# Performance work log

Measured on AMD Instinct MI355X. Metric: run time of the kernel, lower is better.

The kernel has to match this reference:

```python
import jax, jax.numpy as jnp
import numpy as np

# model constants
D = 2048; D_INNER = 4096; H = 64; P = 64; N = 128; K = 4; CHUNK = 256
E = 8; TOPK = 2; I_EXP = 1024; I_SH = 4096
EPS = 1e-5; RES_MULT = 0.22
CONV_DIM = D_INNER + 2 * N  # n_groups=1


def rmsnorm(x, w, eps=EPS):
    var = jnp.mean(x * x, axis=-1, keepdims=True)
    return x * jax.lax.rsqrt(var + eps) * w


def segsum(x):
    # x: [..., L] -> [..., L, L] lower-triangular cumulative sums, -inf above diag
    L = x.shape[-1]
    cs = jnp.cumsum(x, axis=-1)
    d = cs[..., :, None] - cs[..., None, :]
    mask = jnp.tril(jnp.ones((L, L), dtype=bool))
    return jnp.where(mask, d, -jnp.inf)


def ssd(x, dt, A, Bm, Cm, chunk=CHUNK):
    # x:[b,s,h,p] dt:[b,s,h] A:[h] Bm/Cm:[b,s,n] (single group)
    b, S, h, p = x.shape
    n = Bm.shape[-1]
    nc = S // chunk
    xc = x.reshape(b, nc, chunk, h, p)
    dtc = dt.reshape(b, nc, chunk, h)
    Bc = Bm.reshape(b, nc, chunk, n)
    Cc = Cm.reshape(b, nc, chunk, n)
    dA = jnp.transpose(dtc * A, (0, 1, 3, 2))          # [b,c,h,l]
    dA_cum = jnp.cumsum(dA, axis=-1)                    # [b,c,h,l]
    xdt = xc * dtc[..., None]                           # [b,c,l,h,p]
    # intra-chunk (quadratic attention-like block)
    CB = jnp.einsum('bcln,bcsn->bcls', Cc, Bc)
    Lmat = jnp.exp(segsum(dA))                          # [b,c,h,l,s]
    Y = jnp.einsum('bcls,bchls,bcshp->bclhp', CB, Lmat, xdt)
    # per-chunk final states
    decay_states = jnp.exp(dA_cum[..., -1:] - dA_cum)   # [b,c,h,l]
    states = jnp.einsum('bcln,bchl,bclhp->bchpn', Bc, decay_states, xdt)
    # inter-chunk recurrence (small scan over nc chunks)
    chunk_decay = jnp.exp(dA_cum[..., -1])              # [b,c,h]
    dec_c = jnp.moveaxis(chunk_decay, 1, 0)             # [c,b,h]
    st_c = jnp.moveaxis(states, 1, 0)                   # [c,b,h,p,n]

    def step(carry, inp):
        dec, st = inp
        return carry * dec[..., None, None] + st, carry

    _, prev = jax.lax.scan(step, jnp.zeros_like(st_c[0]), (dec_c, st_c))
    prev = jnp.moveaxis(prev, 0, 1)                     # [b,c,h,p,n] state before each chunk
    out_decay = jnp.exp(jnp.transpose(dA_cum, (0, 1, 3, 2)))  # [b,c,l,h]
    Y = Y + jnp.einsum('bcln,bchpn->bclhp', Cc, prev) * out_decay[..., None]
    return Y.reshape(b, S, h, p)


def causal_conv_silu(u, w, bias):
    # u:[b,s,c], depthwise causal conv kernel w:[c,K]
    S = u.shape[1]
    up = jnp.pad(u, ((0, 0), (K - 1, 0), (0, 0)))
    y = sum(up[:, i:i + S, :] * w[:, i] for i in range(K)) + bias
    return jax.nn.silu(y)


def setup_inputs() -> dict:
    key = jax.random.key(0)
    ks = jax.random.split(key, 16)
    B, S = 1, 4096
    sc = 0.02
    return {
        'positions': jnp.arange(B * S, dtype=jnp.int32).reshape(B, S),
        'hidden_states': jax.random.normal(ks[0], (B, S, D), jnp.float32),
        'ln1_w': jnp.ones((D,), jnp.float32),
        'in_proj_w': jax.random.normal(ks[1], (D, 2 * D_INNER + 2 * N + H), jnp.float32) * sc,
        'conv_w': jax.random.normal(ks[2], (CONV_DIM, K), jnp.float32) * 0.2,
        'conv_b': jnp.zeros((CONV_DIM,), jnp.float32),
        'A_log': jnp.log(jax.random.uniform(ks[3], (H,), jnp.float32, 1.0, 16.0)),
        'dt_bias': jax.random.normal(ks[4], (H,), jnp.float32) * 0.5,
        'D_param': jnp.ones((H,), jnp.float32),
        'mamba_norm_w': jnp.ones((D_INNER,), jnp.float32),
        'out_proj_w': jax.random.normal(ks[5], (D_INNER, D), jnp.float32) * sc,
        'ln2_w': jnp.ones((D,), jnp.float32),
        'router_w': jax.random.normal(ks[6], (D, E), jnp.float32) * sc,
        'moe_w_gate_up': jax.random.normal(ks[7], (E, D, 2 * I_EXP), jnp.float32) * sc,
        'moe_w_down': jax.random.normal(ks[8], (E, I_EXP, D), jnp.float32) * sc,
        'shared_w_in': jax.random.normal(ks[9], (D, 2 * I_SH), jnp.float32) * sc,
        'shared_w_out': jax.random.normal(ks[10], (I_SH, D), jnp.float32) * sc,
    }


def reference(positions, hidden_states, ln1_w, in_proj_w, conv_w, conv_b, A_log,
              dt_bias, D_param, mamba_norm_w, out_proj_w, ln2_w, router_w,
              moe_w_gate_up, moe_w_down, shared_w_in, shared_w_out):
    B, S, _ = hidden_states.shape
    residual = hidden_states
    h = rmsnorm(hidden_states, ln1_w)
    # ---- Mamba2 mixer ----
    proj = h @ in_proj_w                                  # [B,S,2*Di+2N+H]
    z = proj[..., :D_INNER]
    xBC = proj[..., D_INNER:D_INNER + CONV_DIM]
    dt_raw = proj[..., D_INNER + CONV_DIM:]
    xBC = causal_conv_silu(xBC, conv_w, conv_b)
    x = xBC[..., :D_INNER].reshape(B, S, H, P)
    Bm = xBC[..., D_INNER:D_INNER + N]
    Cm = xBC[..., D_INNER + N:]
    dt = jax.nn.softplus(dt_raw + dt_bias)                # [B,S,H]
    A = -jnp.exp(A_log)                                   # [H]
    y = ssd(x, dt, A, Bm, Cm) + x * D_param[None, None, :, None]
    y = y.reshape(B, S, D_INNER)
    y = rmsnorm(y * jax.nn.silu(z), mamba_norm_w)         # gated RMSNorm
    mamba_out = y @ out_proj_w
    hidden = residual + mamba_out * RES_MULT
    residual = hidden
    # ---- MoE + shared MLP ----
    h2 = rmsnorm(hidden, ln2_w)
    ht = h2.reshape(-1, D)
    T = ht.shape[0]
    logits = ht @ router_w                                # [T,E]
    topv, topi = jax.lax.top_k(logits, TOPK)
    wts = jax.nn.softmax(topv, axis=-1)
    gates = jnp.zeros((T, E), ht.dtype).at[jnp.arange(T)[:, None], topi].set(wts)
    moe_out = jnp.zeros_like(ht)
    for e in range(E):
        gu = ht @ moe_w_gate_up[e]
        a = jax.nn.silu(gu[:, :I_EXP]) * gu[:, I_EXP:]
        moe_out = moe_out + gates[:, e:e + 1] * (a @ moe_w_down[e])
    gu = ht @ shared_w_in
    shared_out = (jax.nn.silu(gu[:, :I_SH]) * gu[:, I_SH:]) @ shared_w_out
    ff = (moe_out + shared_out).reshape(B, S, D)
    hidden = residual + ff * RES_MULT
    return (hidden, residual)
```

## Files before the change

### kernel.cpp

```cpp
#include <hip/hip_runtime.h>
#include <stdint.h>

typedef unsigned short u16;
typedef __attribute__((ext_vector_type(8))) __bf16 bf16x8;
typedef __attribute__((ext_vector_type(4))) float f32x4;

#define SEQ     4096
#define DMODEL  2048
#define DINNER  4096
#define NHEADS  64
#define HEADP   64
#define NSTATE  128
#define NCHUNK  16
#define CHUNKL  256
#define NPROJ   8512
#define NPROJP  8576
#define CONVDIM 4352
#define RESM    0.22f
#define MAXROWS 9216
#define MAXTILE 72

static __device__ __forceinline__ u16 f2bf(float f){
  union { float f; uint32_t u; } v; v.f = f;
  uint32_t r = v.u + 0x7fffu + ((v.u >> 16) & 1u);
  return (u16)(r >> 16);
}
static __device__ __forceinline__ float bf2f(u16 h){
  union { uint32_t u; float f; } v; v.u = ((uint32_t)h) << 16;
  return v.f;
}
static __device__ __forceinline__ float siluf(float x){ return x / (1.f + __expf(-x)); }

static __device__ __forceinline__ void gll16(const void* g, void* l) {
  __builtin_amdgcn_global_load_lds(
      (const __attribute__((address_space(1))) void*)g,
      (__attribute__((address_space(3))) void*)l, 16, 0, 0);
}

static __device__ __forceinline__ int swz_src_c8(int tid) {
  return ((((tid & 3) - ((tid >> 3) & 3) + 4) & 3) * 8);
}
static __device__ __forceinline__ int swz_rd_sl8(int fr, int g) {
  return (((g + ((fr >> 1) & 3)) & 3) * 8);
}

static __device__ __forceinline__ void decode_tile(
    int id, int NB, int MB, int G, int& bx, int& by)
{
  const int nwg = NB * MB;
  int sid = id;
  if (!(nwg & 7)) {
    const int cpx = nwg >> 3;
    sid = (id & 7) * cpx + (id >> 3);
  }
  const int gsz = MB * G;
  const int fullG = NB / G;
  const int fullCnt = fullG * gsz;
  if (sid < fullCnt) {
    const int grp = sid / gsz;
    const int r = sid - grp * gsz;
    const int q = r / G;
    by = q;
    bx = grp * G + (r - q * G);
  } else {
    const int rem = NB - fullG * G;
    const int r = sid - fullCnt;
    const int q = r / rem;
    by = q;
    bx = fullG * G + (r - q * rem);
  }
}

__global__ __launch_bounds__(256) void rmsnorm_split(
    const float* __restrict__ in, const float* __restrict__ w,
    u16* __restrict__ hi, u16* __restrict__ lo, int width)
{
  const int row = blockIdx.x;
  const float* x = in + (size_t)row * width;
  float ss = 0.f;
  for (int i = threadIdx.x * 4; i < width; i += 1024) {
    float4 v = *(const float4*)&x[i];
    ss += v.x*v.x + v.y*v.y + v.z*v.z + v.w*v.w;
  }
  #pragma unroll
  for (int off = 32; off > 0; off >>= 1) ss += __shfl_down(ss, off);
  __shared__ float red[4];
  if ((threadIdx.x & 63) == 0) red[threadIdx.x >> 6] = ss;
  __syncthreads();
  const float total = red[0] + red[1] + red[2] + red[3];
  const float scale = rsqrtf(total / (float)width + 1e-5f);
  u16* oh = hi + (size_t)row * width;
  u16* ol = lo + (size_t)row * width;
  for (int i = threadIdx.x * 4; i < width; i += 1024) {
    float4 v = *(const float4*)&x[i];
    float4 g = *(const float4*)&w[i];
    #pragma unroll
    for (int q = 0; q < 4; q++) {
      const float val = ((const float*)&v)[q] * scale * ((const float*)&g)[q];
      const u16 H = f2bf(val);
      oh[i+q] = H;
      ol[i+q] = f2bf(val - bf2f(H));
    }
  }
}

__global__ __launch_bounds__(256) void wconv_t(
    const float* __restrict__ W, u16* __restrict__ Bt, int K, int N)
{
  const size_t eo = (size_t)blockIdx.z * K * N;
  W += eo; Bt += eo;
  __shared__ float t[32][33];
  const int n0 = blockIdx.x * 32, k0 = blockIdx.y * 32;
  const int tx = threadIdx.x & 31, ty = threadIdx.x >> 5;
  #pragma unroll
  for (int r = 0; r < 32; r += 8)
    t[ty + r][tx] = W[(size_t)(k0 + ty + r) * N + n0 + tx];
  __syncthreads();
  #pragma unroll
  for (int r = 0; r < 32; r += 8)
    Bt[(size_t)(n0 + ty + r) * K + k0 + tx] = f2bf(t[tx][ty + r]);
}

__global__ __launch_bounds__(256) void wconv_t_glu(
    const float* __restrict__ W, u16* __restrict__ Bt, int K, int N, int H)
{
  const size_t eo = (size_t)blockIdx.z * K * N;
  W += eo; Bt += eo;
  __shared__ float t[32][33];
  const int n0 = blockIdx.x * 32, k0 = blockIdx.y * 32;
  const int tx = threadIdx.x & 31, ty = threadIdx.x >> 5;
  #pragma unroll
  for (int r = 0; r < 32; r += 8)
    t[ty + r][tx] = W[(size_t)(k0 + ty + r) * N + n0 + tx];
  __syncthreads();
  #pragma unroll
  for (int r = 0; r < 32; r += 8) {
    const int n = n0 + ty + r;
    const int orow = (n < H) ? (2 * n) : (2 * (n - H) + 1);
    Bt[(size_t)orow * K + k0 + tx] = f2bf(t[tx][ty + r]);
  }
}

__global__ __launch_bounds__(256) void wconv_t_split(
    const float* __restrict__ W, u16* __restrict__ Bth, u16* __restrict__ Btl, int K, int N)
{
  __shared__ float t[32][33];
  const int n0 = blockIdx.x * 32, k0 = blockIdx.y * 32;
  const int tx = threadIdx.x & 31, ty = threadIdx.x >> 5;
  #pragma unroll
  for (int r = 0; r < 32; r += 8)
    t[ty + r][tx] = W[(size_t)(k0 + ty + r) * N + n0 + tx];
  __syncthreads();
  #pragma unroll
  for (int r = 0; r < 32; r += 8) {
    const float val = t[tx][ty + r];
    const u16 H = f2bf(val);
    const size_t idx = (size_t)(n0 + ty + r) * K + k0 + tx;
    Bth[idx] = H;
    Btl[idx] = f2bf(val - bf2f(H));
  }
}

template<int EPI>
__global__ __launch_bounds__(256, 2) void gemm_bt(
    const u16* __restrict__ A, const u16* __restrict__ Bt,
    float* __restrict__ Cf,
    int Nreal, int K, int ldc, int NB, int MB, int G)
{
  __shared__ u16 As[128 * 32];
  __shared__ u16 Bs[128 * 32];
  int bx, by; decode_tile(blockIdx.x, NB, MB, G, bx, by);
  const int tid = threadIdx.x, lane = tid & 63;
  const int wid = tid >> 6, wr = wid >> 1, wc = wid & 1;
  const int m0 = by * 128, n0 = bx * 128;
  const int fr = lane & 15, g = lane >> 4;
  const int sl8 = swz_rd_sl8(fr, g);
  const f32x4 zero = {0.f, 0.f, 0.f, 0.f};
  f32x4 acc[4][4];
  #pragma unroll
  for (int i = 0; i < 4; i++)
    #pragma unroll
    for (int j = 0; j < 4; j++) acc[i][j] = zero;
  const int c8 = swz_src_c8(tid);
  const u16* pA = A  + (size_t)(m0 + (tid >> 2)) * K + c8;
  const u16* pB = Bt + (size_t)(n0 + (tid >> 2)) * K + c8;
  const size_t rstep = (size_t)64 * K;
  const int l0 = tid * 8;
  for (int k0 = 0; k0 < K; k0 += 32) {
    if (k0) __syncthreads();
    gll16(pA + k0,         &As[l0]);
    gll16(pA + k0 + rstep, &As[2048 + l0]);
    gll16(pB + k0,         &Bs[l0]);
    gll16(pB + k0 + rstep, &Bs[2048 + l0]);
    __syncthreads();
    bf16x8 af[4], bfr[4];
    #pragma unroll
    for (int mi = 0; mi < 4; mi++)
      af[mi] = *(const bf16x8*)&As[(wr * 64 + mi * 16 + fr) * 32 + sl8];
    #pragma unroll
    for (int ni = 0; ni < 4; ni++)
      bfr[ni] = *(const bf16x8*)&Bs[(wc * 64 + ni * 16 + fr) * 32 + sl8];
    #pragma unroll
    for (int mi = 0; mi < 4; mi++)
      #pragma unroll
      for (int ni = 0; ni < 4; ni++)
        acc[mi][ni] = __builtin_amdgcn_mfma_f32_16x16x32_bf16(af[mi], bfr[ni], acc[mi][ni], 0, 0, 0);
  }
  #pragma unroll
  for (int mi = 0; mi < 4; mi++) {
    #pragma unroll
    for (int ni = 0; ni < 4; ni++) {
      const int n = n0 + wc * 64 + ni * 16 + fr;
      if (n >= Nreal) continue;
      #pragma unroll
      for (int i = 0; i < 4; i++) {
        const int m = m0 + wr * 64 + mi * 16 + g * 4 + i;
        Cf[(size_t)m * ldc + n] = acc[mi][ni][i];
      }
    }
  }
}

__global__ __launch_bounds__(256, 2) void gemm_bt_glu(
    const u16* __restrict__ A, const u16* __restrict__ Bt,
    u16* __restrict__ aout,
    int K, int Nhalf, int NB, int MB, int G)
{
  __shared__ u16 As[128 * 32];
  __shared__ u16 Bs[128 * 32];
  int bx, by; decode_tile(blockIdx.x, NB, MB, G, bx, by);
  const int tid = threadIdx.x, lane = tid & 63;
  const int wid = tid >> 6, wr = wid >> 1, wc = wid & 1;
  const int m0 = by * 128, n0 = bx * 128;
  const int fr = lane & 15, g = lane >> 4;
  const int sl8 = swz_rd_sl8(fr, g);
  const f32x4 zero = {0.f, 0.f, 0.f, 0.f};
  f32x4 acc[4][4];
  #pragma unroll
  for (int i = 0; i < 4; i++)
    #pragma unroll
    for (int j = 0; j < 4; j++) acc[i][j] = zero;
  const int c8 = swz_src_c8(tid);
  const u16* pA = A  + (size_t)(m0 + (tid >> 2)) * K + c8;
  const u16* pB = Bt + (size_t)(n0 + (tid >> 2)) * K + c8;
  const size_t rstep = (size_t)64 * K;
  const int l0 = tid * 8;
  for (int k0 = 0; k0 < K; k0 += 32) {
    if (k0) __syncthreads();
    gll16(pA + k0,         &As[l0]);
    gll16(pA + k0 + rstep, &As[2048 + l0]);
    gll16(pB + k0,         &Bs[l0]);
    gll16(pB + k0 + rstep, &Bs[2048 + l0]);
    __syncthreads();
    bf16x8 af[4], bfr[4];
    #pragma unroll
    for (int mi = 0; mi < 4; mi++)
      af[mi] = *(const bf16x8*)&As[(wr * 64 + mi * 16 + fr) * 32 + sl8];
    #pragma unroll
    for (int ni = 0; ni < 4; ni++)
      bfr[ni] = *(const bf16x8*)&Bs[(wc * 64 + ni * 16 + fr) * 32 + sl8];
    #pragma unroll
    for (int mi = 0; mi < 4; mi++)
      #pragma unroll
      for (int ni = 0; ni < 4; ni++)
        acc[mi][ni] = __builtin_amdgcn_mfma_f32_16x16x32_bf16(af[mi], bfr[ni], acc[mi][ni], 0, 0, 0);
  }
  #pragma unroll
  for (int mi = 0; mi < 4; mi++) {
    #pragma unroll
    for (int ni = 0; ni < 4; ni++) {
      const int n = n0 + wc * 64 + ni * 16 + fr;
      #pragma unroll
      for (int i = 0; i < 4; i++) {
        const float v = acc[mi][ni][i];
        const float vp = __shfl_xor(v, 1);
        if (!(fr & 1)) {
          const int m = m0 + wr * 64 + mi * 16 + g * 4 + i;
          aout[(size_t)m * Nhalf + (n >> 1)] = f2bf(siluf(v) * vp);
        }
      }
    }
  }
}

template<int EPI>
__global__ __launch_bounds__(256, 2) void gemm_dd(
    const u16* __restrict__ Ah, const u16* __restrict__ Al,
    const u16* __restrict__ Bh, const u16* __restrict__ Bl,
    float* __restrict__ Cf, const float* __restrict__ res,
    int Nreal, int K, int ldc, float alpha, int NB, int MB, int G)
{
  __shared__ u16 Ash[128 * 32];
  __shared__ u16 Asl[128 * 32];
  __shared__ u16 Bsh[128 * 32];
  __shared__ u16 Bsl[128 * 32];
  int bx, by; decode_tile(blockIdx.x, NB, MB, G, bx, by);
  const int tid = threadIdx.x, lane = tid & 63;
  const int wid = tid >> 6, wr = wid >> 1, wc = wid & 1;
  const int m0 = by * 128, n0 = bx * 128;
  const int fr = lane & 15, g = lane >> 4;
  const int sl8 = swz_rd_sl8(fr, g);
  const f32x4 zero = {0.f, 0.f, 0.f, 0.f};
  f32x4 acc[4][4];
  #pragma unroll
  for (int i = 0; i < 4; i++)
    #pragma unroll
    for (int j = 0; j < 4; j++) acc[i][j] = zero;
  const int c8 = swz_src_c8(tid);
  const size_t offA = (size_t)(m0 + (tid >> 2)) * K + c8;
  const size_t offB = (size_t)(n0 + (tid >> 2)) * K + c8;
  const size_t rstep = (size_t)64 * K;
  const int l0 = tid * 8;
  for (int k0 = 0; k0 < K; k0 += 32) {
    if (k0) __syncthreads();
    gll16(Ah + offA + k0,         &Ash[l0]);
    gll16(Ah + offA + k0 + rstep, &Ash[2048 + l0]);
    gll16(Al + offA + k0,         &Asl[l0]);
    gll16(Al + offA + k0 + rstep, &Asl[2048 + l0]);
    gll16(Bh + offB + k0,         &Bsh[l0]);
    gll16(Bh + offB + k0 + rstep, &Bsh[2048 + l0]);
    gll16(Bl + offB + k0,         &Bsl[l0]);
    gll16(Bl + offB + k0 + rstep, &Bsl[2048 + l0]);
    __syncthreads();
    bf16x8 ah[4], al[4], bh[4], bl[4];
    #pragma unroll
    for (int mi = 0; mi < 4; mi++) {
      const int a = (wr * 64 + mi * 16 + fr) * 32 + sl8;
      ah[mi] = *(const bf16x8*)&Ash[a];
      al[mi] = *(const bf16x8*)&Asl[a];
    }
    #pragma unroll
    for (int ni = 0; ni < 4; ni++) {
      const int b = (wc * 64 + ni * 16 + fr) * 32 + sl8;
      bh[ni] = *(const bf16x8*)&Bsh[b];
      bl[ni] = *(const bf16x8*)&Bsl[b];
    }
    #pragma unroll
    for (int mi = 0; mi < 4; mi++)
      #pragma unroll
      for (int ni = 0; ni < 4; ni++) {
        acc[mi][ni] = __builtin_amdgcn_mfma_f32_16x16x32_bf16(al[mi], bh[ni], acc[mi][ni], 0, 0, 0);
        acc[mi][ni] = __builtin_amdgcn_mfma_f32_16x16x32_bf16(ah[mi], bl[ni], acc[mi][ni], 0, 0, 0);
        acc[mi][ni] = __builtin_amdgcn_mfma_f32_16x16x32_bf16(ah[mi], bh[ni], acc[mi][ni], 0, 0, 0);
      }
  }
  #pragma unroll
  for (int mi = 0; mi < 4; mi++) {
    #pragma unroll
    for (int ni = 0; ni < 4; ni++) {
      const int n = n0 + wc * 64 + ni * 16 + fr;
      if (n >= Nreal) continue;
      #pragma unroll
      for (int i = 0; i < 4; i++) {
        const int m = m0 + wr * 64 + mi * 16 + g * 4 + i;
        const float v = acc[mi][ni][i];
        const size_t idx = (size_t)m * ldc + n;
        if constexpr (EPI == 1) {
          Cf[idx] = res[idx] + alpha * v;
        } else {
          Cf[idx] = v;
        }
      }
    }
  }
}

__global__ __launch_bounds__(256, 2) void gemm_moe_gu(
    const u16* __restrict__ ht, const u16* __restrict__ wGU,
    u16* __restrict__ abufp, const int* __restrict__ tokmap,
    const int* __restrict__ meta)
{
  const int by = blockIdx.y;
  if (by >= meta[24]) return;
  const int e = meta[32 + by];
  const int row0 = meta[104 + by];
  __shared__ u16 As[128 * 32];
  __shared__ u16 Bs[128 * 32];
  const int tid = threadIdx.x, lane = tid & 63;
  const int wid = tid >> 6, wr = wid >> 1, wc = wid & 1;
  const int n0 = blockIdx.x * 128;
  const int fr = lane & 15, g = lane >> 4;
  const int sl8 = swz_rd_sl8(fr, g);
  const f32x4 zero = {0.f, 0.f, 0.f, 0.f};
  f32x4 acc[4][4];
  #pragma unroll
  for (int i = 0; i < 4; i++)
    #pragma unroll
    for (int j = 0; j < 4; j++) acc[i][j] = zero;
  const int r4 = tid >> 2, c8 = swz_src_c8(tid);
  const int tok0 = tokmap[row0 + r4];
  const int tok1 = tokmap[row0 + 64 + r4];
  const u16* pA0 = ht + (size_t)tok0 * DMODEL + c8;
  const u16* pA1 = ht + (size_t)tok1 * DMODEL + c8;
  const u16* pB  = wGU + (size_t)e * 2048 * DMODEL + (size_t)(n0 + r4) * DMODEL + c8;
  const size_t rstep = (size_t)64 * DMODEL;
  const int l0 = tid * 8;
  for (int k0 = 0; k0 < DMODEL; k0 += 32) {
    if (k0) __syncthreads();
    gll16(pA0 + k0,        &As[l0]);
    gll16(pA1 + k0,        &As[2048 + l0]);
    gll16(pB + k0,         &Bs[l0]);
    gll16(pB + k0 + rstep, &Bs[2048 + l0]);
    __syncthreads();
    bf16x8 af[4], bfr[4];
    #pragma unroll
    for (int mi = 0; mi < 4; mi++)
      af[mi] = *(const bf16x8*)&As[(wr * 64 + mi * 16 + fr) * 32 + sl8];
    #pragma unroll
    for (int ni = 0; ni < 4; ni++)
      bfr[ni] = *(const bf16x8*)&Bs[(wc * 64 + ni * 16 + fr) * 32 + sl8];
    #pragma unroll
    for (int mi = 0; mi < 4; mi++)
      #pragma unroll
      for (int ni = 0; ni < 4; ni++)
        acc[mi][ni] = __builtin_amdgcn_mfma_f32_16x16x32_bf16(af[mi], bfr[ni], acc[mi][ni], 0, 0, 0);
  }
  #pragma unroll
  for (int mi = 0; mi < 4; mi++)
    #pragma unroll
    for (int ni = 0; ni < 4; ni++) {
      const int n = n0 + wc * 64 + ni * 16 + fr;
      #pragma unroll
      for (int i = 0; i < 4; i++) {
        const float v = acc[mi][ni][i];
        const float vp = __shfl_xor(v, 1);
        if (!(fr & 1)) {
          const int m = row0 + wr * 64 + mi * 16 + g * 4 + i;
          abufp[(size_t)m * 1024 + (n >> 1)] = f2bf(siluf(v) * vp);
        }
      }
    }
}

__global__ __launch_bounds__(256, 2) void gemm_moe_down(
    const u16* __restrict__ abuf, const u16* __restrict__ wDN,
    u16* __restrict__ dout, const float* __restrict__ gatew,
    const int* __restrict__ meta)
{
  const int by = blockIdx.y;
  if (by >= meta[24]) return;
  const int e = meta[32 + by];
  const int row0 = meta[104 + by];
  __shared__ u16 As[128 * 32];
  __shared__ u16 Bs[128 * 32];
  const int tid = threadIdx.x, lane = tid & 63;
  const int wid = tid >> 6, wr = wid >> 1, wc = wid & 1;
  const int n0 = blockIdx.x * 128;
  const int fr = lane & 15, g = lane >> 4;
  const int sl8 = swz_rd_sl8(fr, g);
  const f32x4 zero = {0.f, 0.f, 0.f, 0.f};
  f32x4 acc[4][4];
  #pragma unroll
  for (int i = 0; i < 4; i++)
    #pragma unroll
    for (int j = 0; j < 4; j++) acc[i][j] = zero;
  const int r4 = tid >> 2, c8 = swz_src_c8(tid);
  const u16* pA = abuf + (size_t)(row0 + r4) * 1024 + c8;
  const u16* pB = wDN + (size_t)e * 1024 * 2048 + (size_t)(n0 + r4) * 1024 + c8;
  const size_t rstepA = (size_t)64 * 1024;
  const int l0 = tid * 8;
  for (int k0 = 0; k0 < 1024; k0 += 32) {
    if (k0) __syncthreads();
    gll16(pA + k0,          &As[l0]);
    gll16(pA + k0 + rstepA, &As[2048 + l0]);
    gll16(pB + k0,          &Bs[l0]);
    gll16(pB + k0 + rstepA, &Bs[2048 + l0]);
    __syncthreads();
    bf16x8 af[4], bfr[4];
    #pragma unroll
    for (int mi = 0; mi < 4; mi++)
      af[mi] = *(const bf16x8*)&As[(wr * 64 + mi * 16 + fr) * 32 + sl8];
    #pragma unroll
    for (int ni = 0; ni < 4; ni++)
      bfr[ni] = *(const bf16x8*)&Bs[(wc * 64 + ni * 16 + fr) * 32 + sl8];
    #pragma unroll
    for (int mi = 0; mi < 4; mi++)
      #pragma unroll
      for (int ni = 0; ni < 4; ni++)
        acc[mi][ni] = __builtin_amdgcn_mfma_f32_16x16x32_bf16(af[mi], bfr[ni], acc[mi][ni], 0, 0, 0);
  }
  #pragma unroll
  for (int mi = 0; mi < 4; mi++)
    #pragma unroll
    for (int ni = 0; ni < 4; ni++) {
      const int n = n0 + wc * 64 + ni * 16 + fr;
      #pragma unroll
      for (int i = 0; i < 4; i++) {
        const int m = row0 + wr * 64 + mi * 16 + g * 4 + i;
        dout[(size_t)m * 2048 + n] = f2bf(acc[mi][ni][i] * gatew[m]);
      }
    }
}

__global__ __launch_bounds__(256) void conv_silu_dt(
    const float* __restrict__ proj, const float* __restrict__ cw, const float* __restrict__ cb,
    const float* __restrict__ dt_bias,
    float* __restrict__ x, float* __restrict__ Bc, float* __restrict__ Cc,
    float* __restrict__ dt)
{
  const int c = blockIdx.x * 256 + threadIdx.x;
  const int s = blockIdx.y;
  if (c < CONVDIM) {
    const float4 w = *(const float4*)&cw[c * 4];
    float acc = cb[c];
    const float* pc = proj + (size_t)DINNER + c;
    if (s >= 3) acc += pc[(size_t)(s-3) * NPROJP] * w.x;
    if (s >= 2) acc += pc[(size_t)(s-2) * NPROJP] * w.y;
    if (s >= 1) acc += pc[(size_t)(s-1) * NPROJP] * w.z;
    acc += pc[(size_t)s * NPROJP] * w.w;
    const float v = siluf(acc);
    if (c < DINNER)                 x[(size_t)s * DINNER + c] = v;
    else if (c < DINNER + NSTATE)   Bc[(size_t)s * NSTATE + (c - DINNER)] = v;
    else                            Cc[(size_t)s * NSTATE + (c - DINNER - NSTATE)] = v;
  } else if (c < CONVDIM + 64) {
    const int h = c - CONVDIM;
    const float v = proj[(size_t)s * NPROJP + (DINNER + CONVDIM) + h] + dt_bias[h];
    dt[(size_t)s * 64 + h] = fmaxf(v, 0.f) + log1pf(__expf(-fabsf(v)));
  }
}

__global__ __launch_bounds__(64) void ssd_cum_seq(
    const float* __restrict__ dt, const float* __restrict__ A_log,
    float* __restrict__ cum, float* __restrict__ cdec)
{
  const int c = blockIdx.x, h = threadIdx.x;
  const float A = -__expf(A_log[h]);
  float run = 0.f;
  float* co = cum + ((size_t)(c * 64 + h)) * 256;
  const float* dp = dt + (size_t)c * 256 * 64 + h;
  #pragma unroll 4
  for (int l = 0; l < 256; l++) {
    run += dp[(size_t)l * 64] * A;
    co[l] = run;
  }
  cdec[c * 64 + h] = __expf(run);
}

__global__ __launch_bounds__(256) void ssd_cb(
    const float* __restrict__ Cc, const float* __restrict__ Bc, float* __restrict__ CBt)
{
  const int c = blockIdx.y;
  const int lt = blockIdx.x >> 2, st = blockIdx.x & 3;
  if (st > lt) return;
  __shared__ float Cn[128][64];
  __shared__ float Bn[128][64];
  const int tid = threadIdx.x;
  #pragma unroll
  for (int rep = 0; rep < 8; rep++) {
    const int lin = rep * 1024 + tid * 4;
    const int r = lin >> 7, cc = lin & 127;
    float4 cv = *(const float4*)&Cc[((size_t)(c*256 + lt*64 + r)) * 128 + cc];
    float4 bv = *(const float4*)&Bc[((size_t)(c*256 + st*64 + r)) * 128 + cc];
    Cn[cc+0][r] = cv.x; Cn[cc+1][r] = cv.y; Cn[cc+2][r] = cv.z; Cn[cc+3][r] = cv.w;
    Bn[cc+0][r] = bv.x; Bn[cc+1][r] = bv.y; Bn[cc+2][r] = bv.z; Bn[cc+3][r] = bv.w;
  }
  __syncthreads();
  const int lb = (tid >> 4) * 4, sb = (tid & 15) * 4;
  float acc[4][4] = {};
  for (int n = 0; n < 128; n++) {
    float cv[4], bv[4];
    #pragma unroll
    for (int i = 0; i < 4; i++) { cv[i] = Cn[n][lb+i]; bv[i] = Bn[n][sb+i]; }
    #pragma unroll
    for (int i = 0; i < 4; i++)
      #pragma unroll
      for (int j = 0; j < 4; j++) acc[i][j] += cv[i] * bv[j];
  }
  #pragma unroll
  for (int is = 0; is < 4; is++) {
    const int sg = st*64 + sb + is;
    float4 o; o.x = acc[0][is]; o.y = acc[1][is]; o.z = acc[2][is]; o.w = acc[3][is];
    *(float4*)&CBt[((size_t)(c*256 + sg)) * 256 + lt*64 + lb] = o;
  }
}

__global__ __launch_bounds__(256, 2) void ssd_intra_mfma(
    const float* __restrict__ x, const float* __restrict__ dt, const float* __restrict__ cum,
    const float* __restrict__ CBt, float* __restrict__ Yw)
{
  const int c = blockIdx.x, h = blockIdx.y;
  const int tid = threadIdx.x, lane = tid & 63, w = tid >> 6;
  const int fr = lane & 15, g = lane >> 4;
  __shared__ float cumL[256];
  __shared__ u16 Ph[256 * 32], Pl[256 * 32];
  __shared__ u16 Xh[64 * 32],  Xl[64 * 32];
  cumL[tid] = cum[((size_t)(c*64 + h)) * 256 + tid];
  const f32x4 zero = {0.f, 0.f, 0.f, 0.f};
  f32x4 acc[4][4];
  #pragma unroll
  for (int i = 0; i < 4; i++)
    #pragma unroll
    for (int j = 0; j < 4; j++) acc[i][j] = zero;
  const size_t cb0 = (size_t)c * 65536;
  for (int ts = 0; ts < 8; ts++) {
    __syncthreads();
    {
      const int sl = tid >> 3, p0 = (tid & 7) * 8;
      const int sg = c*256 + ts*32 + sl;
      const float dtv = dt[(size_t)sg * 64 + h];
      const float* xr = x + (size_t)sg * DINNER + h*64 + p0;
      const float4 v0 = *(const float4*)&xr[0];
      const float4 v1 = *(const float4*)&xr[4];
      #pragma unroll
      for (int q = 0; q < 8; q++) {
        const float v = ((q < 4) ? ((const float*)&v0)[q] : ((const float*)&v1)[q-4]) * dtv;
        const u16 H = f2bf(v);
        Xh[(p0 + q) * 32 + sl] = H;
        Xl[(p0 + q) * 32 + sl] = f2bf(v - bf2f(H));
      }
    }
    {
      const int l = tid;
      const float myc = cumL[l];
      #pragma unroll 4
      for (int j = 0; j < 32; j++) {
        const int s = ts*32 + j;
        const float cb = CBt[cb0 + (size_t)s * 256 + l];
        float p = 0.f;
        if (s <= l) p = cb * __expf(myc - cumL[s]);
        const u16 H = f2bf(p);
        Ph[l * 32 + j] = H;
        Pl[l * 32 + j] = f2bf(p - bf2f(H));
      }
    }
    __syncthreads();
    if (ts * 32 < (w + 1) * 64) {
      bf16x8 ah[4], al[4], bh[4], bl[4];
      #pragma unroll
      for (int mi = 0; mi < 4; mi++) {
        const int a = (w*64 + mi*16 + fr) * 32 + g*8;
        ah[mi] = *(const bf16x8*)&Ph[a];
        al[mi] = *(const bf16x8*)&Pl[a];
      }
      #pragma unroll
      for (int ni = 0; ni < 4; ni++) {
        const int b = (ni*16 + fr) * 32 + g*8;
        bh[ni] = *(const bf16x8*)&Xh[b];
        bl[ni] = *(const bf16x8*)&Xl[b];
      }
      #pragma unroll
      for (int mi = 0; mi < 4; mi++)
        #pragma unroll
        for (int ni = 0; ni < 4; ni++) {
          acc[mi][ni] = __builtin_amdgcn_mfma_f32_16x16x32_bf16(al[mi], bl[ni], acc[mi][ni], 0, 0, 0);
          acc[mi][ni] = __builtin_amdgcn_mfma_f32_16x16x32_bf16(al[mi], bh[ni], acc[mi][ni], 0, 0, 0);
          acc[mi][ni] = __builtin_amdgcn_mfma_f32_16x16x32_bf16(ah[mi], bl[ni], acc[mi][ni], 0, 0, 0);
          acc[mi][ni] = __builtin_amdgcn_mfma_f32_16x16x32_bf16(ah[mi], bh[ni], acc[mi][ni], 0, 0, 0);
        }
    }
  }
  #pragma unroll
  for (int mi = 0; mi < 4; mi++)
    #pragma unroll
    for (int ni = 0; ni < 4; ni++)
      #pragma unroll
      for (int i = 0; i < 4; i++) {
        const int l = w*64 + mi*16 + g*4 + i;
        const int p = ni*16 + fr;
        Yw[(size_t)(c*256 + l) * DINNER + h*64 + p] = acc[mi][ni][i];
      }
}

__global__ __launch_bounds__(256, 2) void ssd_states_mfma(
    const float* __restrict__ x, const float* __restrict__ Bc, const float* __restrict__ dt,
    const float* __restrict__ cum, float* __restrict__ states)
{
  const int c = blockIdx.x, h = blockIdx.y;
  const int tid = threadIdx.x, lane = tid & 63, w = tid >> 6;
  const int fr = lane & 15, g = lane >> 4;
  __shared__ float cd[256];
  __shared__ u16 Xth[64 * 32],  Xtl[64 * 32];
  __shared__ u16 Bth[128 * 32], Btl[128 * 32];
  {
    const float* cumh = cum + ((size_t)(c*64 + h)) * 256;
    cd[tid] = __expf(cumh[255] - cumh[tid]) * dt[(size_t)(c*256 + tid) * 64 + h];
  }
  const f32x4 zero = {0.f, 0.f, 0.f, 0.f};
  f32x4 acc[4][2];
  #pragma unroll
  for (int i = 0; i < 4; i++) { acc[i][0] = zero; acc[i][1] = zero; }
  for (int lt = 0; lt < 8; lt++) {
    __syncthreads();
    {
      const int ll = tid >> 3, p0 = (tid & 7) * 8;
      const int lg = c*256 + lt*32 + ll;
      const float cdv = cd[lt*32 + ll];
      const float* xr = x + (size_t)lg * DINNER + h*64 + p0;
      const float4 v0 = *(const float4*)&xr[0];
      const float4 v1 = *(const float4*)&xr[4];
      #pragma unroll
      for (int q = 0; q < 8; q++) {
        const float v = ((q < 4) ? ((const float*)&v0)[q] : ((const float*)&v1)[q-4]) * cdv;
        const u16 H = f2bf(v);
        Xth[(p0 + q) * 32 + ll] = H;
        Xtl[(p0 + q) * 32 + ll] = f2bf(v - bf2f(H));
      }
    }
    {
      const int ll = tid >> 3, n0 = (tid & 7) * 16;
      const float* br = Bc + (size_t)(c*256 + lt*32 + ll) * 128 + n0;
      #pragma unroll
      for (int q4 = 0; q4 < 4; q4++) {
        const float4 bv = *(const float4*)&br[q4*4];
        #pragma unroll
        for (int q = 0; q < 4; q++) {
          const float v = ((const float*)&bv)[q];
          const u16 H = f2bf(v);
          Bth[(n0 + q4*4 + q) * 32 + ll] = H;
          Btl[(n0 + q4*4 + q) * 32 + ll] = f2bf(v - bf2f(H));
        }
      }
    }
    __syncthreads();
    bf16x8 ah[4], al[4], bh[2], bl[2];
    #pragma unroll
    for (int mi = 0; mi < 4; mi++) {
      const int a = (mi*16 + fr) * 32 + g*8;
      ah[mi] = *(const bf16x8*)&Xth[a];
      al[mi] = *(const bf16x8*)&Xtl[a];
    }
    #pragma unroll
    for (int ni = 0; ni < 2; ni++) {
      const int b = (w*32 + ni*16 + fr) * 32 + g*8;
      bh[ni] = *(const bf16x8*)&Bth[b];
      bl[ni] = *(const bf16x8*)&Btl[b];
    }
    #pragma unroll
    for (int mi = 0; mi < 4; mi++)
      #pragma unroll
      for (int ni = 0; ni < 2; ni++) {
        acc[mi][ni] = __builtin_amdgcn_mfma_f32_16x16x32_bf16(al[mi], bl[ni], acc[mi][ni], 0, 0, 0);
        acc[mi][ni] = __builtin_amdgcn_mfma_f32_16x16x32_bf16(al[mi], bh[ni], acc[mi][ni], 0, 0, 0);
        acc[mi][ni] = __builtin_amdgcn_mfma_f32_16x16x32_bf16(ah[mi], bl[ni], acc[mi][ni], 0, 0, 0);
        acc[mi][ni] = __builtin_amdgcn_mfma_f32_16x16x32_bf16(ah[mi], bh[ni], acc[mi][ni], 0, 0, 0);
      }
  }
  #pragma unroll
  for (int mi = 0; mi < 4; mi++)
    #pragma unroll
    for (int ni = 0; ni < 2; ni++)
      #pragma unroll
      for (int i = 0; i < 4; i++) {
        const int p = mi*16 + g*4 + i;
        const int n = w*32 + ni*16 + fr;
        states[(((size_t)(c*64 + h)) * 64 + p) * 128 + n] = acc[mi][ni][i];
      }
}

__global__ void ssd_scan(
    const float* __restrict__ states, const float* __restrict__ cdec, float* __restrict__ prev)
{
  const int hp = blockIdx.x;
  const int n = threadIdx.x;
  const int h = hp >> 6;
  float carry = 0.f;
  for (int c = 0; c < NCHUNK; c++) {
    const size_t idx = ((size_t)c * 4096 + hp) * 128 + n;
    prev[idx] = carry;
    carry = carry * cdec[c*64 + h] + states[idx];
  }
}

__global__ __launch_bounds__(256, 2) void ssd_final_mfma(
    const float* __restrict__ Cc, const float* __restrict__ prev, const float* __restrict__ cum,
    const float* __restrict__ x, const float* __restrict__ proj, const float* __restrict__ Dp,
    float* __restrict__ Yw)
{
  const int c = blockIdx.x, h = blockIdx.y;
  const int tid = threadIdx.x, lane = tid & 63, w = tid >> 6;
  const int fr = lane & 15, g = lane >> 4;
  __shared__ float cumL[256];
  __shared__ u16 Ch[256 * 32], Cl[256 * 32];
  __shared__ u16 Pvh[64 * 32], Pvl[64 * 32];
  cumL[tid] = cum[((size_t)(c*64 + h)) * 256 + tid];
  const f32x4 zero = {0.f, 0.f, 0.f, 0.f};
  f32x4 acc[4][4];
  #pragma unroll
  for (int i = 0; i < 4; i++)
    #pragma unroll
    for (int j = 0; j < 4; j++) acc[i][j] = zero;
  for (int nt = 0; nt < 4; nt++) {
    __syncthreads();
    {
      #pragma unroll
      for (int rep = 0; rep < 32; rep++) {
        const int l = rep*8 + (tid >> 5);
        const int j = tid & 31;
        const float v = Cc[(size_t)(c*256 + l) * 128 + nt*32 + j];
        const u16 H = f2bf(v);
        Ch[l*32 + j] = H;
        Cl[l*32 + j] = f2bf(v - bf2f(H));
      }
    }
    {
      const int p = tid >> 2, q0 = (tid & 3) * 8;
      const float* pr = prev + ((size_t)c * 4096 + h*64 + p) * 128 + nt*32 + q0;
      const float4 v0 = *(const float4*)&pr[0];
      const float4 v1 = *(const float4*)&pr[4];
      #pragma unroll
      for (int q = 0; q < 8; q++) {
        const float v = (q < 4) ? ((const float*)&v0)[q] : ((const float*)&v1)[q-4];
        const u16 H = f2bf(v);
        Pvh[p*32 + q0 + q] = H;
        Pvl[p*32 + q0 + q] = f2bf(v - bf2f(H));
      }
    }
    __syncthreads();
    bf16x8 ah[4], al[4], bh[4], bl[4];
    #pragma unroll
    for (int mi = 0; mi < 4; mi++) {
      const int a = (w*64 + mi*16 + fr) * 32 + g*8;
      ah[mi] = *(const bf16x8*)&Ch[a];
      al[mi] = *(const bf16x8*)&Cl[a];
    }
    #pragma unroll
    for (int ni = 0; ni < 4; ni++) {
      const int b = (ni*16 + fr) * 32 + g*8;
      bh[ni] = *(const bf16x8*)&Pvh[b];
      bl[ni] = *(const bf16x8*)&Pvl[b];
    }
    #pragma unroll
    for (int mi = 0; mi < 4; mi++)
      #pragma unroll
      for (int ni = 0; ni < 4; ni++) {
        acc[mi][ni] = __builtin_amdgcn_mfma_f32_16x16x32_bf16(al[mi], bl[ni], acc[mi][ni], 0, 0, 0);
        acc[mi][ni] = __builtin_amdgcn_mfma_f32_16x16x32_bf16(al[mi], bh[ni], acc[mi][ni], 0, 0, 0);
        acc[mi][ni] = __builtin_amdgcn_mfma_f32_16x16x32_bf16(ah[mi], bl[ni], acc[mi][ni], 0, 0, 0);
        acc[mi][ni] = __builtin_amdgcn_mfma_f32_16x16x32_bf16(ah[mi], bh[ni], acc[mi][ni], 0, 0, 0);
      }
  }
  const float Dv = Dp[h];
  #pragma unroll
  for (int mi = 0; mi < 4; mi++) {
    #pragma unroll
    for (int i = 0; i < 4; i++) {
      const int l = w*64 + mi*16 + g*4 + i;
      const float odec = __expf(cumL[l]);
      const size_t rowo = (size_t)(c*256 + l);
      #pragma unroll
      for (int ni = 0; ni < 4; ni++) {
        const int p = ni*16 + fr;
        const size_t iy = rowo * DINNER + h*64 + p;
        const float yv = Yw[iy] + acc[mi][ni][i] * odec + Dv * x[iy];
        const float z = proj[rowo * NPROJP + h*64 + p];
        Yw[iy] = yv * siluf(z);
      }
    }
  }
}

__global__ __launch_bounds__(256) void router_norm(
    const float* __restrict__ h2, const float* __restrict__ ln2w,
    const float* __restrict__ rw, u16* __restrict__ ht,
    int* __restrict__ eidx, float* __restrict__ ew)
{
  const int t = blockIdx.x;
  const float* xr = h2 + (size_t)t * DMODEL;
  float ss = 0.f;
  for (int i = threadIdx.x * 4; i < DMODEL; i += 1024) {
    float4 v = *(const float4*)&xr[i];
    ss += v.x*v.x + v.y*v.y + v.z*v.z + v.w*v.w;
  }
  #pragma unroll
  for (int off = 32; off > 0; off >>= 1) ss += __shfl_down(ss, off);
  __shared__ float red[4];
  if ((threadIdx.x & 63) == 0) red[threadIdx.x >> 6] = ss;
  __syncthreads();
  const float scale = rsqrtf((red[0]+red[1]+red[2]+red[3]) / (float)DMODEL + 1e-5f);
  float acc[8];
  #pragma unroll
  for (int j = 0; j < 8; j++) acc[j] = 0.f;
  u16* o = ht + (size_t)t * DMODEL;
  for (int i = threadIdx.x; i < DMODEL; i += 256) {
    const float v = xr[i] * scale * ln2w[i];
    o[i] = f2bf(v);
    const float* r = rw + (size_t)i * 8;
    #pragma unroll
    for (int j = 0; j < 8; j++) acc[j] += v * r[j];
  }
  #pragma unroll
  for (int j = 0; j < 8; j++)
    #pragma unroll
    for (int off = 32; off > 0; off >>= 1) acc[j] += __shfl_down(acc[j], off);
  __shared__ float rbuf[4][8];
  if ((threadIdx.x & 63) == 0)
    #pragma unroll
    for (int j = 0; j < 8; j++) rbuf[threadIdx.x >> 6][j] = acc[j];
  __syncthreads();
  if (threadIdx.x == 0) {
    float lg[8];
    #pragma unroll
    for (int j = 0; j < 8; j++) lg[j] = rbuf[0][j]+rbuf[1][j]+rbuf[2][j]+rbuf[3][j];
    int i1 = 0;
    #pragma unroll
    for (int j = 1; j < 8; j++) if (lg[j] > lg[i1]) i1 = j;
    int i2 = -1;
    #pragma unroll
    for (int j = 0; j < 8; j++) if (j != i1 && (i2 < 0 || lg[j] > lg[i2])) i2 = j;
    const float e2 = __expf(lg[i2] - lg[i1]);
    const float inv = 1.f / (1.f + e2);
    eidx[t*2]   = i1;  ew[t*2]   = inv;
    eidx[t*2+1] = i2;  ew[t*2+1] = e2 * inv;
  }
}

__global__ void moe_zero(int* __restrict__ tokmap, int* __restrict__ meta)
{
  const int i = blockIdx.x * 256 + threadIdx.x;
  if (i < MAXROWS) tokmap[i] = 0;
  if (i < 16) meta[i] = 0;
}

__global__ void moe_count(const int* __restrict__ eidx, int* __restrict__ meta)
{
  const int i = blockIdx.x * 256 + threadIdx.x;
  if (i < SEQ * 2) atomicAdd(&meta[eidx[i]], 1);
}

__global__ void moe_offsets(int* __restrict__ meta)
{
  if (threadIdx.x != 0 || blockIdx.x != 0) return;
  int off = 0, T = 0;
  for (int e = 0; e < 8; e++) {
    meta[16 + e] = off;
    const int nt = (meta[e] + 127) >> 7;
    for (int j = 0; j < nt; j++) {
      meta[32 + T] = e;
      meta[104 + T] = off + j * 128;
      T++;
    }
    off += nt * 128;
  }
  meta[24] = T;
}

__global__ void moe_place(
    const int* __restrict__ eidx, const float* __restrict__ ew,
    int* __restrict__ meta, int* __restrict__ tokmap,
    float* __restrict__ gatew, int* __restrict__ posmap)
{
  const int i = blockIdx.x * 256 + threadIdx.x;
  if (i >= SEQ * 2) return;
  const int e = eidx[i];
  const int pos = atomicAdd(&meta[8 + e], 1);
  const int r = meta[16 + e] + pos;
  tokmap[r] = i >> 1;
  gatew[r] = ew[i];
  posmap[i] = r;
}

__global__ __launch_bounds__(256) void final_moe(
    const float* __restrict__ h2, const float* __restrict__ shout,
    const u16* __restrict__ dout, const int* __restrict__ posmap,
    float* __restrict__ o)
{
  const int t = blockIdx.x;
  const int p0 = posmap[t*2], p1 = posmap[t*2+1];
  const u16* d0 = dout + (size_t)p0 * 2048 + threadIdx.x * 8;
  const u16* d1 = dout + (size_t)p1 * 2048 + threadIdx.x * 8;
  const size_t base = (size_t)t * 2048 + threadIdx.x * 8;
  #pragma unroll
  for (int q = 0; q < 8; q++) {
    const float ff = shout[base + q] + bf2f(d0[q]) + bf2f(d1[q]);
    o[base + q] = h2[base + q] + RESM * ff;
  }
}

#define OFF_WAH   ((size_t)0)
#define OFF_WAL   ((size_t)35127296)
#define OFF_PROJ  ((size_t)70254592)
#define OFF_X     ((size_t)210763776)
#define OFF_Y     ((size_t)277872640)
#define OFF_HP    ((size_t)344981504)
#define OFF_BC    ((size_t)378535936)
#define OFF_CC    ((size_t)380633088)
#define OFF_DT    ((size_t)382730240)
#define OFF_CUM   ((size_t)383778816)
#define OFF_CDEC  ((size_t)384827392)
#define OFF_CB    ((size_t)384831488)

extern "C" void kernel_launch(void* const* d_in, const int* in_sizes, int n_in,
                              void* d_out, int out_size, void* d_ws, size_t ws_size,
                              hipStream_t stream)
{
  const float* hs       = (const float*)d_in[1];
  const float* ln1_w    = (const float*)d_in[2];
  const float* w_inproj = (const float*)d_in[3];
  const float* conv_w   = (const float*)d_in[4];
  const float* conv_b   = (const float*)d_in[5];
  const float* A_log    = (const float*)d_in[6];
  const float* dt_bias  = (const float*)d_in[7];
  const float* D_param  = (const float*)d_in[8];
  const float* mnorm_w  = (const float*)d_in[9];
  const float* w_outp   = (const float*)d_in[10];
  const float* ln2_w    = (const float*)d_in[11];
  const float* router_w = (const float*)d_in[12];
  const float* w_gu     = (const float*)d_in[13];
  const float* w_down   = (const float*)d_in[14];
  const float* w_shin   = (const float*)d_in[15];
  const float* w_shout  = (const float*)d_in[16];

  char* ws = (char*)d_ws;
  u16*   wAh    = (u16*)(ws + OFF_WAH);
  u16*   wAl    = (u16*)(ws + OFF_WAL);
  float* projf  = (float*)(ws + OFF_PROJ);
  float* xbuf   = (float*)(ws + OFF_X);
  float* ybuf   = (float*)(ws + OFF_Y);
  float* Bcb    = (float*)(ws + OFF_BC);
  float* Ccb    = (float*)(ws + OFF_CC);
  float* dtb    = (float*)(ws + OFF_DT);
  float* cumb   = (float*)(ws + OFF_CUM);
  float* cdecb  = (float*)(ws + OFF_CDEC);
  float* cbt    = (float*)(ws + OFF_CB);

  u16*   hhi    = (u16*)(ws + OFF_HP);
  u16*   hlo    = (u16*)(ws + OFF_HP + 16777216);
  float* prevb  = (float*)(ws + OFF_HP);
  u16*   wDN    = (u16*)(ws + OFF_HP);
  float* stbuf  = (float*)(ws + OFF_WAH);
  u16*   ynhi   = (u16*)(ws + OFF_WAH);
  u16*   ynlo   = (u16*)(ws + OFF_WAL);
  u16*   wBh    = (u16*)(ws + OFF_PROJ);
  u16*   wBl    = (u16*)(ws + OFF_PROJ + 16777216);
  u16*   wE     = (u16*)(ws + OFF_WAH);
  u16*   wD     = (u16*)(ws + OFF_WAH + 33554432);
  u16*   wGU    = (u16*)(ws + OFF_WAH);
  u16*   abufp  = (u16*)(ws + OFF_PROJ + 83886080);
  u16*   ht     = (u16*)(ws + OFF_X);
  u16*   ash    = (u16*)(ws + OFF_X + 16777216);
  u16*   dout   = (u16*)(ws + OFF_X + 16777216);
  float* shout  = (float*)(ws + OFF_Y);

  int*   eidx   = (int*)(ws + OFF_BC);
  float* ew     = (float*)(ws + OFF_BC + 65536);
  int*   posmap = (int*)(ws + OFF_BC + 131072);
  int*   tokmap = (int*)(ws + OFF_BC + 196608);
  float* gatew  = (float*)(ws + OFF_BC + 262144);
  int*   meta   = (int*)(ws + OFF_BC + 327680);

  float* out0    = (float*)d_out;
  float* hidden2 = out0 + (size_t)SEQ * DMODEL;

  rmsnorm_split<<<SEQ, 256, 0, stream>>>(hs, ln1_w, hhi, hlo, DMODEL);
  wconv_t_split<<<dim3(NPROJ/32, DMODEL/32), 256, 0, stream>>>(w_inproj, wAh, wAl, DMODEL, NPROJ);
  gemm_dd<3><<<67*32, 256, 0, stream>>>(hhi, hlo, wAh, wAl, projf, nullptr,
                                        NPROJ, DMODEL, NPROJP, 0.f, 67, 32, 4);
  conv_silu_dt<<<dim3(18, SEQ), 256, 0, stream>>>(projf, conv_w, conv_b, dt_bias,
                                                  xbuf, Bcb, Ccb, dtb);
  ssd_cum_seq<<<NCHUNK, 64, 0, stream>>>(dtb, A_log, cumb, cdecb);
  ssd_cb<<<dim3(16, NCHUNK), 256, 0, stream>>>(Ccb, Bcb, cbt);
  ssd_intra_mfma<<<dim3(NCHUNK, NHEADS), 256, 0, stream>>>(xbuf, dtb, cumb, cbt, ybuf);
  ssd_states_mfma<<<dim3(NCHUNK, NHEADS), 256, 0, stream>>>(xbuf, Bcb, dtb, cumb, stbuf);
  ssd_scan<<<NHEADS*HEADP, 128, 0, stream>>>(stbuf, cdecb, prevb);
  ssd_final_mfma<<<dim3(NCHUNK, NHEADS), 256, 0, stream>>>(Ccb, prevb, cumb, xbuf, projf, D_param, ybuf);
  rmsnorm_split<<<SEQ, 256, 0, stream>>>(ybuf, mnorm_w, ynhi, ynlo, DINNER);
  wconv_t_split<<<dim3(DMODEL/32, DINNER/32), 256, 0, stream>>>(w_outp, wBh, wBl, DINNER, DMODEL);
  gemm_dd<1><<<16*32, 256, 0, stream>>>(ynhi, ynlo, wBh, wBl, hidden2, hs,
                                        DMODEL, DINNER, DMODEL, RESM, 16, 32, 4);

  router_norm<<<SEQ, 256, 0, stream>>>(hidden2, ln2_w, router_w, ht, eidx, ew);
  moe_zero<<<(MAXROWS+255)/256, 256, 0, stream>>>(tokmap, meta);
  moe_count<<<SEQ*2/256, 256, 0, stream>>>(eidx, meta);
  moe_offsets<<<1, 64, 0, stream>>>(meta);
  moe_place<<<SEQ*2/256, 256, 0, stream>>>(eidx, ew, meta, tokmap, gatew, posmap);

  wconv_t_glu<<<dim3(8192/32, DMODEL/32), 256, 0, stream>>>(w_shin, wE, DMODEL, 8192, 4096);
  gemm_bt_glu<<<64*32, 256, 0, stream>>>(ht, wE, ash, DMODEL, 4096, 64, 32, 4);
  wconv_t<<<dim3(DMODEL/32, 4096/32), 256, 0, stream>>>(w_shout, wD, 4096, DMODEL);
  gemm_bt<3><<<16*32, 256, 0, stream>>>(ash, wD, shout, DMODEL, 4096, DMODEL, 16, 32, 4);

  wconv_t_glu<<<dim3(2048/32, DMODEL/32, 8), 256, 0, stream>>>(w_gu, wGU, DMODEL, 2048, 1024);
  wconv_t<<<dim3(DMODEL/32, 1024/32, 8), 256, 0, stream>>>(w_down, wDN, 1024, DMODEL);
  gemm_moe_gu<<<dim3(16, MAXTILE), 256, 0, stream>>>(ht, wGU, abufp, tokmap, meta);
  gemm_moe_down<<<dim3(16, MAXTILE), 256, 0, stream>>>(abufp, wDN, dout, gatew, meta);

  final_moe<<<SEQ, 256, 0, stream>>>(hidden2, shout, dout, posmap, out0);
}
```

Measured before the change: 1.806 ms.

## Raise GEMM occupancy, drop lo*lo MFMA terms, merge MoE routing kernels

Raises the launch-bounds occupancy hint from 2 to 3 blocks per CU on all GEMM and SSD MFMA kernels. This trades register budget for more resident waves, with a risk of spills. It also drops the low-by-low bf16 split product in the three SSD MFMA kernels, cutting a quarter of their MFMAs at a small precision cost. The four MoE routing kernels are fused into one single-block kernel using shared-memory atomics, which removes launch overhead and global atomics but serializes the work on one CU.

```diff
diff --git a/kernel.cpp b/kernel.cpp
--- a/kernel.cpp
+++ b/kernel.cpp
@@ -162,7 +162,7 @@
 }
 
 template<int EPI>
-__global__ __launch_bounds__(256, 2) void gemm_bt(
+__global__ __launch_bounds__(256, 3) void gemm_bt(
     const u16* __restrict__ A, const u16* __restrict__ Bt,
     float* __restrict__ Cf,
     int Nreal, int K, int ldc, int NB, int MB, int G)
@@ -221,7 +221,7 @@
   }
 }
 
-__global__ __launch_bounds__(256, 2) void gemm_bt_glu(
+__global__ __launch_bounds__(256, 3) void gemm_bt_glu(
     const u16* __restrict__ A, const u16* __restrict__ Bt,
     u16* __restrict__ aout,
     int K, int Nhalf, int NB, int MB, int G)
@@ -284,7 +284,7 @@
 }
 
 template<int EPI>
-__global__ __launch_bounds__(256, 2) void gemm_dd(
+__global__ __launch_bounds__(256, 3) void gemm_dd(
     const u16* __restrict__ Ah, const u16* __restrict__ Al,
     const u16* __restrict__ Bh, const u16* __restrict__ Bl,
     float* __restrict__ Cf, const float* __restrict__ res,
@@ -365,7 +365,7 @@
   }
 }
 
-__global__ __launch_bounds__(256, 2) void gemm_moe_gu(
+__global__ __launch_bounds__(256, 3) void gemm_moe_gu(
     const u16* __restrict__ ht, const u16* __restrict__ wGU,
     u16* __restrict__ abufp, const int* __restrict__ tokmap,
     const int* __restrict__ meta)
@@ -432,7 +432,7 @@
     }
 }
 
-__global__ __launch_bounds__(256, 2) void gemm_moe_down(
+__global__ __launch_bounds__(256, 3) void gemm_moe_down(
     const u16* __restrict__ abuf, const u16* __restrict__ wDN,
     u16* __restrict__ dout, const float* __restrict__ gatew,
     const int* __restrict__ meta)
@@ -574,7 +574,7 @@
   }
 }
 
-__global__ __launch_bounds__(256, 2) void ssd_intra_mfma(
+__global__ __launch_bounds__(256, 3) void ssd_intra_mfma(
     const float* __restrict__ x, const float* __restrict__ dt, const float* __restrict__ cum,
     const float* __restrict__ CBt, float* __restrict__ Yw)
 {
@@ -642,7 +642,6 @@
       for (int mi = 0; mi < 4; mi++)
         #pragma unroll
         for (int ni = 0; ni < 4; ni++) {
-          acc[mi][ni] = __builtin_amdgcn_mfma_f32_16x16x32_bf16(al[mi], bl[ni], acc[mi][ni], 0, 0, 0);
           acc[mi][ni] = __builtin_amdgcn_mfma_f32_16x16x32_bf16(al[mi], bh[ni], acc[mi][ni], 0, 0, 0);
           acc[mi][ni] = __builtin_amdgcn_mfma_f32_16x16x32_bf16(ah[mi], bl[ni], acc[mi][ni], 0, 0, 0);
           acc[mi][ni] = __builtin_amdgcn_mfma_f32_16x16x32_bf16(ah[mi], bh[ni], acc[mi][ni], 0, 0, 0);
@@ -661,7 +660,7 @@
       }
 }
 
-__global__ __launch_bounds__(256, 2) void ssd_states_mfma(
+__global__ __launch_bounds__(256, 3) void ssd_states_mfma(
     const float* __restrict__ x, const float* __restrict__ Bc, const float* __restrict__ dt,
     const float* __restrict__ cum, float* __restrict__ states)
 {
@@ -729,7 +728,6 @@
     for (int mi = 0; mi < 4; mi++)
       #pragma unroll
       for (int ni = 0; ni < 2; ni++) {
-        acc[mi][ni] = __builtin_amdgcn_mfma_f32_16x16x32_bf16(al[mi], bl[ni], acc[mi][ni], 0, 0, 0);
         acc[mi][ni] = __builtin_amdgcn_mfma_f32_16x16x32_bf16(al[mi], bh[ni], acc[mi][ni], 0, 0, 0);
         acc[mi][ni] = __builtin_amdgcn_mfma_f32_16x16x32_bf16(ah[mi], bl[ni], acc[mi][ni], 0, 0, 0);
         acc[mi][ni] = __builtin_amdgcn_mfma_f32_16x16x32_bf16(ah[mi], bh[ni], acc[mi][ni], 0, 0, 0);
@@ -761,7 +759,7 @@
   }
 }
 
-__global__ __launch_bounds__(256, 2) void ssd_final_mfma(
+__global__ __launch_bounds__(256, 3) void ssd_final_mfma(
     const float* __restrict__ Cc, const float* __restrict__ prev, const float* __restrict__ cum,
     const float* __restrict__ x, const float* __restrict__ proj, const float* __restrict__ Dp,
     float* __restrict__ Yw)
@@ -823,7 +821,6 @@
     for (int mi = 0; mi < 4; mi++)
       #pragma unroll
       for (int ni = 0; ni < 4; ni++) {
-        acc[mi][ni] = __builtin_amdgcn_mfma_f32_16x16x32_bf16(al[mi], bl[ni], acc[mi][ni], 0, 0, 0);
         acc[mi][ni] = __builtin_amdgcn_mfma_f32_16x16x32_bf16(al[mi], bh[ni], acc[mi][ni], 0, 0, 0);
         acc[mi][ni] = __builtin_amdgcn_mfma_f32_16x16x32_bf16(ah[mi], bl[ni], acc[mi][ni], 0, 0, 0);
         acc[mi][ni] = __builtin_amdgcn_mfma_f32_16x16x32_bf16(ah[mi], bh[ni], acc[mi][ni], 0, 0, 0);
@@ -904,49 +901,44 @@
   }
 }
 
-__global__ void moe_zero(int* __restrict__ tokmap, int* __restrict__ meta)
-{
-  const int i = blockIdx.x * 256 + threadIdx.x;
-  if (i < MAXROWS) tokmap[i] = 0;
-  if (i < 16) meta[i] = 0;
-}
-
-__global__ void moe_count(const int* __restrict__ eidx, int* __restrict__ meta)
-{
-  const int i = blockIdx.x * 256 + threadIdx.x;
-  if (i < SEQ * 2) atomicAdd(&meta[eidx[i]], 1);
-}
-
-__global__ void moe_offsets(int* __restrict__ meta)
-{
-  if (threadIdx.x != 0 || blockIdx.x != 0) return;
-  int off = 0, T = 0;
-  for (int e = 0; e < 8; e++) {
-    meta[16 + e] = off;
-    const int nt = (meta[e] + 127) >> 7;
-    for (int j = 0; j < nt; j++) {
-      meta[32 + T] = e;
-      meta[104 + T] = off + j * 128;
-      T++;
-    }
-    off += nt * 128;
-  }
-  meta[24] = T;
-}
-
-__global__ void moe_place(
+__global__ __launch_bounds__(1024) void moe_route(
     const int* __restrict__ eidx, const float* __restrict__ ew,
-    int* __restrict__ meta, int* __restrict__ tokmap,
-    float* __restrict__ gatew, int* __restrict__ posmap)
-{
-  const int i = blockIdx.x * 256 + threadIdx.x;
-  if (i >= SEQ * 2) return;
-  const int e = eidx[i];
-  const int pos = atomicAdd(&meta[8 + e], 1);
-  const int r = meta[16 + e] + pos;
-  tokmap[r] = i >> 1;
-  gatew[r] = ew[i];
-  posmap[i] = r;
+    int* __restrict__ tokmap, float* __restrict__ gatew,
+    int* __restrict__ posmap, int* __restrict__ meta)
+{
+  const int tid = threadIdx.x;
+  __shared__ int cnt[8], base[8];
+  if (tid < 8) cnt[tid] = 0;
+  for (int i = tid; i < MAXROWS; i += 1024) tokmap[i] = 0;
+  __syncthreads();
+  for (int i = tid; i < SEQ * 2; i += 1024)
+    atomicAdd(&cnt[eidx[i]], 1);
+  __syncthreads();
+  if (tid == 0) {
+    int off = 0, T = 0;
+    for (int e = 0; e < 8; e++) {
+      base[e] = off;
+      meta[16 + e] = off;
+      const int nt = (cnt[e] + 127) >> 7;
+      for (int j = 0; j < nt; j++) {
+        meta[32 + T] = e;
+        meta[104 + T] = off + j * 128;
+        T++;
+      }
+      off += nt * 128;
+      cnt[e] = 0;
+    }
+    meta[24] = T;
+  }
+  __syncthreads();
+  for (int i = tid; i < SEQ * 2; i += 1024) {
+    const int e = eidx[i];
+    const int pos = atomicAdd(&cnt[e], 1);
+    const int r = base[e] + pos;
+    tokmap[r] = i >> 1;
+    gatew[r] = ew[i];
+    posmap[i] = r;
+  }
 }
 
 __global__ __launch_bounds__(256) void final_moe(
@@ -1059,10 +1051,7 @@
                                         DMODEL, DINNER, DMODEL, RESM, 16, 32, 4);
 
   router_norm<<<SEQ, 256, 0, stream>>>(hidden2, ln2_w, router_w, ht, eidx, ew);
-  moe_zero<<<(MAXROWS+255)/256, 256, 0, stream>>>(tokmap, meta);
-  moe_count<<<SEQ*2/256, 256, 0, stream>>>(eidx, meta);
-  moe_offsets<<<1, 64, 0, stream>>>(meta);
-  moe_place<<<SEQ*2/256, 256, 0, stream>>>(eidx, ew, meta, tokmap, gatew, posmap);
+  moe_route<<<1, 1024, 0, stream>>>(eidx, ew, tokmap, gatew, posmap, meta);
 
   wconv_t_glu<<<dim3(8192/32, DMODEL/32), 256, 0, stream>>>(w_shin, wE, DMODEL, 8192, 4096);
   gemm_bt_glu<<<64*32, 256, 0, stream>>>(ht, wE, ash, DMODEL, 4096, 64, 32, 4);
```

Measured after the change: 1.926 ms. 6.7% more time.
